# Optimization experiments

Hardware: AMD Instinct MI355X
Metric: run time of the kernel (lower is better)

## Reference

```python
import jax, jax.numpy as jnp
import numpy as np

B, N = 4, 128
INPUT_SIZE, Z_SIZE = 512, 256
D_TENSOR, N_HEADS, SEQ_LEN = 64, 8, 64
D = D_TENSOR * N_HEADS * SEQ_LEN  # 32768


def setup_inputs() -> dict:
    key = jax.random.key(0)
    ks = jax.random.split(key, 10)
    s = lambda fan_in: 1.0 / np.sqrt(fan_in)
    return {
        "x": jax.random.normal(ks[0], (B, N, INPUT_SIZE), dtype=jnp.float32),
        "z": jax.random.normal(ks[1], (B, N, Z_SIZE), dtype=jnp.float32),
        "Wq": jax.random.uniform(ks[2], (Z_SIZE, D), jnp.float32, -s(Z_SIZE), s(Z_SIZE)),
        "bq": jax.random.uniform(ks[3], (D,), jnp.float32, -s(Z_SIZE), s(Z_SIZE)),
        "Wk": jax.random.uniform(ks[4], (INPUT_SIZE, D), jnp.float32, -s(INPUT_SIZE), s(INPUT_SIZE)),
        "bk": jax.random.uniform(ks[5], (D,), jnp.float32, -s(INPUT_SIZE), s(INPUT_SIZE)),
        "Wv": jax.random.uniform(ks[6], (INPUT_SIZE, D), jnp.float32, -s(INPUT_SIZE), s(INPUT_SIZE)),
        "bv": jax.random.uniform(ks[7], (D,), jnp.float32, -s(INPUT_SIZE), s(INPUT_SIZE)),
        "Wo": jax.random.uniform(ks[8], (D, INPUT_SIZE), jnp.float32, -s(D), s(D)),
        "bo": jax.random.uniform(ks[9], (INPUT_SIZE,), jnp.float32, -s(D), s(D)),
    }


def reference(x, z, Wq, bq, Wk, bk, Wv, bv, Wo, bo):
    # Q, K, V: [B, N, heads, seq_len, d_tensor]
    Q = (z @ Wq + bq).reshape(B, N, N_HEADS, SEQ_LEN, D_TENSOR)
    K = (x @ Wk + bk).reshape(B, N, N_HEADS, SEQ_LEN, D_TENSOR)
    V = (x @ Wv + bv).reshape(B, N, N_HEADS, SEQ_LEN, D_TENSOR)
    scores = jnp.einsum("bnhqd,bnhkd->bnhqk", Q, K) / np.sqrt(D_TENSOR).astype(np.float32)
    attn = jax.nn.softmax(scores, axis=-1)
    out = jnp.einsum("bnhqk,bnhkd->bnhqd", attn, V).reshape(B, N, D)
    return out @ Wo + bo
```

## Files before the change

kernel.cpp:

```cpp
#include <hip/hip_runtime.h>
#include <stdint.h>


typedef __attribute__((ext_vector_type(8))) short short8;
typedef __attribute__((ext_vector_type(4))) float floatx4;

__device__ __forceinline__ unsigned short f2bf(float f) {
  union { float f; unsigned int u; } v; v.f = f;
  unsigned int u = v.u + 0x7FFFu + ((v.u >> 16) & 1u);
  return (unsigned short)(u >> 16);
}

__device__ __forceinline__ unsigned int cvt_pk_bf16(float lo, float hi) {
  unsigned int r;
  asm("v_cvt_pk_bf16_f32 %0, %1, %2" : "=v"(r) : "v"(lo), "v"(hi));
  return r;
}

#define MFMA16(a, b, c) __builtin_amdgcn_mfma_f32_16x16x32_bf16((a), (b), (c), 0, 0, 0)

#define STAGE_TILE(SRC, LD, LDSARR)                                            \
  do {                                                                         \
    _Pragma("unroll") for (int i_ = 0; i_ < 4; ++i_) {                         \
      int e_ = tid + (i_ << 8);                                                \
      int r_ = e_ >> 3;                                                        \
      int c_ = (e_ & 7) ^ (r_ & 7);                                            \
      __builtin_amdgcn_global_load_lds(                                        \
          (const __attribute__((address_space(1))) unsigned int*)((SRC) +      \
              (size_t)r_ * (LD) + (c_ << 3)),                                  \
          (__attribute__((address_space(3))) unsigned int*)(&(LDSARR)[e_ << 3]),\
          16, 0, 0);                                                           \
    }                                                                          \
  } while (0)

#define FRAG(LDSARR, ROW, KS)                                                  \
  (*(const short8*)(&(LDSARR)[(((ROW) << 6)) +                                 \
      ((((((KS) << 2) + quad)) ^ ((ROW) & 7)) << 3)]))

template <int LDW>
__device__ __forceinline__ void b_issue(const float* __restrict__ Wp,
                                        float* fB, int n, int octb) {
#pragma unroll
  for (int g = 0; g < 4; ++g) {
    const int oct = octb + 2 * g;
    const float* src = Wp + (size_t)(oct << 3) * LDW + n;
#pragma unroll
    for (int j = 0; j < 8; ++j) fB[g * 8 + j] = src[(size_t)j * LDW];
  }
}

__device__ __forceinline__ void b_write(unsigned short* Bs, const float* fB,
                                        int n, int octb) {
#pragma unroll
  for (int g = 0; g < 4; ++g) {
    const int oct = octb + 2 * g;
    uint4 p;
    p.x = cvt_pk_bf16(fB[g * 8 + 0], fB[g * 8 + 1]);
    p.y = cvt_pk_bf16(fB[g * 8 + 2], fB[g * 8 + 3]);
    p.z = cvt_pk_bf16(fB[g * 8 + 4], fB[g * 8 + 5]);
    p.w = cvt_pk_bf16(fB[g * 8 + 6], fB[g * 8 + 7]);
    *(uint4*)(&Bs[(n << 6) + ((oct ^ (n & 7)) << 3)]) = p;
  }
}

__global__ __launch_bounds__(256) void convert_xz(const float* __restrict__ x,
                                                  const float* __restrict__ z,
                                                  unsigned short* __restrict__ xb,
                                                  unsigned short* __restrict__ zb) {
  int idx = (blockIdx.x * 256 + threadIdx.x) * 8;
  const float* src;
  unsigned short* dst;
  if (idx < 262144) { src = x + idx; dst = xb + idx; }
  else              { src = z + (idx - 262144); dst = zb + (idx - 262144); }
  float4 f0 = *(const float4*)src;
  float4 f1 = *(const float4*)(src + 4);
  uint4 p;
  p.x = f2bf(f0.x) | ((unsigned)f2bf(f0.y) << 16);
  p.y = f2bf(f0.z) | ((unsigned)f2bf(f0.w) << 16);
  p.z = f2bf(f1.x) | ((unsigned)f2bf(f1.y) << 16);
  p.w = f2bf(f1.z) | ((unsigned)f2bf(f1.w) << 16);
  *(uint4*)dst = p;
}

__global__ __launch_bounds__(256, 2) void gemm_qkv(const unsigned short* __restrict__ xb,
                                                   const unsigned short* __restrict__ zb,
                                                   const float* __restrict__ Wq,
                                                   const float* __restrict__ Wk,
                                                   const float* __restrict__ Wv,
                                                   const float* __restrict__ bq,
                                                   const float* __restrict__ bk,
                                                   const float* __restrict__ bv,
                                                   unsigned short* __restrict__ Qb,
                                                   unsigned short* __restrict__ Kb,
                                                   unsigned short* __restrict__ Vb) {
  __shared__ __align__(16) unsigned short As[2][128 * 64];
  __shared__ __align__(16) unsigned short Bs[2][128 * 64];
  const int tid = threadIdx.x;
  const int zsel = blockIdx.z;
  const unsigned short* A;
  const float* W;
  const float* bias;
  unsigned short* C;
  int Ka;
  if (zsel == 0)      { A = zb; W = Wq; bias = bq; C = Qb; Ka = 256; }
  else if (zsel == 1) { A = xb; W = Wk; bias = bk; C = Kb; Ka = 512; }
  else                { A = xb; W = Wv; bias = bv; C = Vb; Ka = 512; }
  const int id = blockIdx.x;
  const int xcd = id & 7, bj = id >> 3;
  const int m0 = (bj & 3) << 7;
  const int n0 = ((xcd << 5) | (bj >> 2)) << 7;
  const int lane = tid & 63, wid = tid >> 6;
  const int quad = lane >> 4, l15 = lane & 15;
  const int wm = wid >> 1, wn = wid & 1;
  const int n = tid & 127;
  const int octb = __builtin_amdgcn_readfirstlane(tid >> 7);
  const int nsteps = Ka >> 6;

  float fB[32];
  floatx4 acc[4][4] = {};
  int c = 0;
  STAGE_TILE(A + (size_t)m0 * Ka, Ka, As[0]);
  b_issue<32768>(W + n0, fB, n, octb);
  for (int t = 0; t < nsteps; ++t) {
    b_write(Bs[c], fB, n, octb);
    __syncthreads();
    if (t + 1 < nsteps) {
      STAGE_TILE(A + (size_t)m0 * Ka + ((t + 1) << 6), Ka, As[c ^ 1]);
      b_issue<32768>(W + ((size_t)(t + 1) << 6) * 32768 + n0, fB, n, octb);
    }
    __builtin_amdgcn_sched_barrier(0);
#pragma unroll
    for (int ks = 0; ks < 2; ++ks) {
      short8 aF[4], bF[4];
#pragma unroll
      for (int mi = 0; mi < 4; ++mi) aF[mi] = FRAG(As[c], wm * 64 + mi * 16 + l15, ks);
#pragma unroll
      for (int ni = 0; ni < 4; ++ni) bF[ni] = FRAG(Bs[c], wn * 64 + ni * 16 + l15, ks);
#pragma unroll
      for (int mi = 0; mi < 4; ++mi)
#pragma unroll
        for (int ni = 0; ni < 4; ++ni)
          acc[mi][ni] = MFMA16(aF[mi], bF[ni], acc[mi][ni]);
    }
    c ^= 1;
  }
#pragma unroll
  for (int ni = 0; ni < 4; ++ni) {
    int col = n0 + wn * 64 + ni * 16 + l15;
    float bv2 = bias[col];
#pragma unroll
    for (int mi = 0; mi < 4; ++mi) {
      int row = m0 + wm * 64 + mi * 16 + (quad << 2);
#pragma unroll
      for (int r = 0; r < 4; ++r)
        C[(size_t)(row + r) * 32768 + col] = f2bf(acc[mi][ni][r] + bv2);
    }
  }
}

__global__ __launch_bounds__(256) void attn64(const unsigned short* __restrict__ Qb,
                                              const unsigned short* __restrict__ Kb,
                                              const unsigned short* __restrict__ Vb,
                                              unsigned short* __restrict__ Ob) {
  __shared__ __align__(16) unsigned short Qs[64 * 72];
  __shared__ __align__(16) unsigned short Ks[64 * 72];
  __shared__ __align__(16) unsigned short VT[64 * 72];
  __shared__ __align__(16) unsigned short Ps[64 * 72];
  const int tid = threadIdx.x;
  const int bn = blockIdx.x >> 3, h = blockIdx.x & 7;
  const size_t base = (size_t)bn * 32768 + (size_t)h * 4096;
  const unsigned short* q = Qb + base;
  const unsigned short* k = Kb + base;
  const unsigned short* v = Vb + base;
#pragma unroll
  for (int i = 0; i < 2; ++i) {
    int e = tid + (i << 8);
    int r = e >> 3, dblk = e & 7;
    *(uint4*)(&Qs[r * 72 + dblk * 8]) = *(const uint4*)(q + r * 64 + dblk * 8);
    *(uint4*)(&Ks[r * 72 + dblk * 8]) = *(const uint4*)(k + r * 64 + dblk * 8);
    uint4 vv = *(const uint4*)(v + r * 64 + dblk * 8);
    const unsigned short* pv = (const unsigned short*)&vv;
#pragma unroll
    for (int j = 0; j < 8; ++j)
      VT[(dblk * 8 + j) * 72 + r] = pv[j];
  }
  __syncthreads();
  const int lane = tid & 63, wid = tid >> 6;
  const int quad = lane >> 4, l15 = lane & 15;
  const int qs = wid << 4;
  short8 aq0 = *(const short8*)(&Qs[(qs + l15) * 72 + quad * 8]);
  short8 aq1 = *(const short8*)(&Qs[(qs + l15) * 72 + 32 + quad * 8]);
  floatx4 s[4] = {};
#pragma unroll
  for (int ni = 0; ni < 4; ++ni) {
    short8 b0 = *(const short8*)(&Ks[(ni * 16 + l15) * 72 + quad * 8]);
    short8 b1 = *(const short8*)(&Ks[(ni * 16 + l15) * 72 + 32 + quad * 8]);
    s[ni] = MFMA16(aq0, b0, s[ni]);
    s[ni] = MFMA16(aq1, b1, s[ni]);
  }
#pragma unroll
  for (int r = 0; r < 4; ++r) {
    float e0 = s[0][r] * 0.125f, e1 = s[1][r] * 0.125f;
    float e2 = s[2][r] * 0.125f, e3 = s[3][r] * 0.125f;
    float m = fmaxf(fmaxf(e0, e1), fmaxf(e2, e3));
    m = fmaxf(m, __shfl_xor(m, 1));
    m = fmaxf(m, __shfl_xor(m, 2));
    m = fmaxf(m, __shfl_xor(m, 4));
    m = fmaxf(m, __shfl_xor(m, 8));
    float x0 = __expf(e0 - m), x1 = __expf(e1 - m);
    float x2 = __expf(e2 - m), x3 = __expf(e3 - m);
    float t = x0 + x1 + x2 + x3;
    t += __shfl_xor(t, 1); t += __shfl_xor(t, 2);
    t += __shfl_xor(t, 4); t += __shfl_xor(t, 8);
    float inv = __builtin_amdgcn_rcpf(t);
    int row = qs + (quad << 2) + r;
    Ps[row * 72 +      l15] = f2bf(x0 * inv);
    Ps[row * 72 + 16 + l15] = f2bf(x1 * inv);
    Ps[row * 72 + 32 + l15] = f2bf(x2 * inv);
    Ps[row * 72 + 48 + l15] = f2bf(x3 * inv);
  }
  __syncthreads();
  short8 ap0 = *(const short8*)(&Ps[(qs + l15) * 72 + quad * 8]);
  short8 ap1 = *(const short8*)(&Ps[(qs + l15) * 72 + 32 + quad * 8]);
  floatx4 o[4] = {};
#pragma unroll
  for (int ni = 0; ni < 4; ++ni) {
    short8 b0 = *(const short8*)(&VT[(ni * 16 + l15) * 72 + quad * 8]);
    short8 b1 = *(const short8*)(&VT[(ni * 16 + l15) * 72 + 32 + quad * 8]);
    o[ni] = MFMA16(ap0, b0, o[ni]);
    o[ni] = MFMA16(ap1, b1, o[ni]);
  }
  unsigned short* outp = Ob + base;
#pragma unroll
  for (int ni = 0; ni < 4; ++ni)
#pragma unroll
    for (int r = 0; r < 4; ++r)
      outp[(qs + (quad << 2) + r) * 64 + ni * 16 + l15] = f2bf(o[ni][r]);
}

__global__ __launch_bounds__(256, 2) void gemm_out(const unsigned short* __restrict__ A,
                                                   const float* __restrict__ Wo,
                                                   float* __restrict__ Cp) {
  __shared__ __align__(16) unsigned short As[2][128 * 64];
  __shared__ __align__(16) unsigned short Bs[2][128 * 64];
  const int tid = threadIdx.x;
  const int id = blockIdx.x;
  const int xcd = id & 7, bj = id >> 3;
  const int m0 = (bj & 3) << 7;
  const int q = bj >> 2;
  const int n0 = (q & 3) << 7;
  const int ks = (xcd << 2) | (q >> 2);
  const int kbase = ks << 10;
  const int lane = tid & 63, wid = tid >> 6;
  const int quad = lane >> 4, l15 = lane & 15;
  const int wm = wid >> 1, wn = wid & 1;
  const int n = tid & 127;
  const int octb = __builtin_amdgcn_readfirstlane(tid >> 7);

  float fB[32];
  floatx4 acc[4][4] = {};
  int c = 0;
  STAGE_TILE(A + (size_t)m0 * 32768 + kbase, 32768, As[0]);
  b_issue<512>(Wo + (size_t)kbase * 512 + n0, fB, n, octb);
  for (int t = 0; t < 16; ++t) {
    b_write(Bs[c], fB, n, octb);
    __syncthreads();
    if (t + 1 < 16) {
      STAGE_TILE(A + (size_t)m0 * 32768 + kbase + ((t + 1) << 6), 32768, As[c ^ 1]);
      b_issue<512>(Wo + (size_t)(kbase + ((t + 1) << 6)) * 512 + n0, fB, n, octb);
    }
    __builtin_amdgcn_sched_barrier(0);
#pragma unroll
    for (int kss = 0; kss < 2; ++kss) {
      short8 aF[4], bF[4];
#pragma unroll
      for (int mi = 0; mi < 4; ++mi) aF[mi] = FRAG(As[c], wm * 64 + mi * 16 + l15, kss);
#pragma unroll
      for (int ni = 0; ni < 4; ++ni) bF[ni] = FRAG(Bs[c], wn * 64 + ni * 16 + l15, kss);
#pragma unroll
      for (int mi = 0; mi < 4; ++mi)
#pragma unroll
        for (int ni = 0; ni < 4; ++ni)
          acc[mi][ni] = MFMA16(aF[mi], bF[ni], acc[mi][ni]);
    }
    c ^= 1;
  }
  float* outp = Cp + (size_t)ks * 262144;
#pragma unroll
  for (int ni = 0; ni < 4; ++ni) {
    int col = n0 + wn * 64 + ni * 16 + l15;
#pragma unroll
    for (int mi = 0; mi < 4; ++mi) {
      int row = m0 + wm * 64 + mi * 16 + (quad << 2);
#pragma unroll
      for (int r = 0; r < 4; ++r)
        outp[(size_t)(row + r) * 512 + col] = acc[mi][ni][r];
    }
  }
}

__global__ __launch_bounds__(256) void reduce_out(const float* __restrict__ Cp,
                                                  const float* __restrict__ bias,
                                                  float* __restrict__ C) {
  int idx = blockIdx.x * 256 + threadIdx.x;
  float s = bias[idx & 511];
#pragma unroll
  for (int k = 0; k < 32; ++k) s += Cp[(size_t)k * 262144 + idx];
  C[idx] = s;
}

extern "C" void kernel_launch(void* const* d_in, const int* in_sizes, int n_in,
                              void* d_out, int out_size, void* d_ws, size_t ws_size,
                              hipStream_t stream) {
  const float* x  = (const float*)d_in[0];
  const float* z  = (const float*)d_in[1];
  const float* Wq = (const float*)d_in[2];
  const float* bq = (const float*)d_in[3];
  const float* Wk = (const float*)d_in[4];
  const float* bk = (const float*)d_in[5];
  const float* Wv = (const float*)d_in[6];
  const float* bv = (const float*)d_in[7];
  const float* Wo = (const float*)d_in[8];
  const float* bo = (const float*)d_in[9];
  float* out = (float*)d_out;
  char* ws = (char*)d_ws;

  unsigned short* Qb = (unsigned short*)(ws + 0);
  unsigned short* Kb = (unsigned short*)(ws + 33554432);
  unsigned short* Vb = (unsigned short*)(ws + 67108864);
  unsigned short* Ob = (unsigned short*)(ws + 100663296);
  unsigned short* xb = (unsigned short*)(ws + 134217728);
  unsigned short* zb = (unsigned short*)(ws + 134742016);
  float*          Cp = (float*)(ws + 135266304);

  convert_xz<<<dim3(192), 256, 0, stream>>>(x, z, xb, zb);

  gemm_qkv<<<dim3(1024, 1, 3), 256, 0, stream>>>(xb, zb, Wq, Wk, Wv,
                                                 bq, bk, bv, Qb, Kb, Vb);

  attn64<<<dim3(4096), 256, 0, stream>>>(Qb, Kb, Vb, Ob);

  gemm_out<<<dim3(512), 256, 0, stream>>>(Ob, Wo, Cp);

  reduce_out<<<dim3(1024), 256, 0, stream>>>(Cp, bo, out);
}
```

Measured before the change: 350.3 us.

## Double-buffer weight register prefetch with explicit waitcnt in both GEMMs

Both GEMM kernels now keep two register buffers of FP32 weights and prefetch the weight tile two k-steps ahead, unrolling the loop by two with static LDS buffers. Explicit s_waitcnt vmcnt/lgkmcnt plus a raw s_barrier replace __syncthreads, and sched_barriers pin the order of loads and MFMAs. The goal is to hide global weight-load latency behind MFMA work. The cost is 32 more VGPRs per thread, which could hurt occupancy under launch_bounds(256,2), and correctness now depends on the hand-written vmcnt counts matching the real number of loads.

```diff
diff --git a/kernel.cpp b/kernel.cpp
--- a/kernel.cpp
+++ b/kernel.cpp
@@ -93,8 +93,8 @@
                                                    unsigned short* __restrict__ Qb,
                                                    unsigned short* __restrict__ Kb,
                                                    unsigned short* __restrict__ Vb) {
-  __shared__ __align__(16) unsigned short As[2][128 * 64];
-  __shared__ __align__(16) unsigned short Bs[2][128 * 64];
+  __shared__ __align__(16) unsigned short As0[128 * 64], As1[128 * 64];
+  __shared__ __align__(16) unsigned short Bs0[128 * 64], Bs1[128 * 64];
   const int tid = threadIdx.x;
   const int zsel = blockIdx.z;
   const unsigned short* A;
@@ -116,33 +116,49 @@
   const int octb = __builtin_amdgcn_readfirstlane(tid >> 7);
   const int nsteps = Ka >> 6;
 
-  float fB[32];
+  float fB0[32], fB1[32];
   floatx4 acc[4][4] = {};
-  int c = 0;
-  STAGE_TILE(A + (size_t)m0 * Ka, Ka, As[0]);
-  b_issue<32768>(W + n0, fB, n, octb);
-  for (int t = 0; t < nsteps; ++t) {
-    b_write(Bs[c], fB, n, octb);
-    __syncthreads();
-    if (t + 1 < nsteps) {
-      STAGE_TILE(A + (size_t)m0 * Ka + ((t + 1) << 6), Ka, As[c ^ 1]);
-      b_issue<32768>(W + ((size_t)(t + 1) << 6) * 32768 + n0, fB, n, octb);
-    }
+
+  b_issue<32768>(W + n0, fB0, n, octb);
+  __builtin_amdgcn_sched_barrier(0);
+  STAGE_TILE(A + (size_t)m0 * Ka, Ka, As0);
+  __builtin_amdgcn_sched_barrier(0);
+  b_issue<32768>(W + (size_t)64 * 32768 + n0, fB1, n, octb);
+  __builtin_amdgcn_sched_barrier(0);
+
+  auto step = [&](int t, float (&fBc)[32], unsigned short* AsC,
+                  unsigned short* BsC, unsigned short* AsN) {
+    if (t == nsteps - 1) { asm volatile("s_waitcnt vmcnt(0)" ::: "memory"); }
+    else                 { asm volatile("s_waitcnt vmcnt(32)" ::: "memory"); }
+    __builtin_amdgcn_sched_barrier(0);
+    b_write(BsC, fBc, n, octb);
+    asm volatile("s_waitcnt lgkmcnt(0)" ::: "memory");
+    __builtin_amdgcn_s_barrier();
+    __builtin_amdgcn_sched_barrier(0);
+    if (t + 1 < nsteps)
+      STAGE_TILE(A + (size_t)m0 * Ka + ((t + 1) << 6), Ka, AsN);
     __builtin_amdgcn_sched_barrier(0);
 #pragma unroll
     for (int ks = 0; ks < 2; ++ks) {
       short8 aF[4], bF[4];
 #pragma unroll
-      for (int mi = 0; mi < 4; ++mi) aF[mi] = FRAG(As[c], wm * 64 + mi * 16 + l15, ks);
-#pragma unroll
-      for (int ni = 0; ni < 4; ++ni) bF[ni] = FRAG(Bs[c], wn * 64 + ni * 16 + l15, ks);
+      for (int mi = 0; mi < 4; ++mi) aF[mi] = FRAG(AsC, wm * 64 + mi * 16 + l15, ks);
+#pragma unroll
+      for (int ni = 0; ni < 4; ++ni) bF[ni] = FRAG(BsC, wn * 64 + ni * 16 + l15, ks);
 #pragma unroll
       for (int mi = 0; mi < 4; ++mi)
 #pragma unroll
         for (int ni = 0; ni < 4; ++ni)
           acc[mi][ni] = MFMA16(aF[mi], bF[ni], acc[mi][ni]);
     }
-    c ^= 1;
+    __builtin_amdgcn_sched_barrier(0);
+    if (t + 2 < nsteps)
+      b_issue<32768>(W + ((size_t)(t + 2) << 6) * 32768 + n0, fBc, n, octb);
+    __builtin_amdgcn_sched_barrier(0);
+  };
+  for (int t = 0; t < nsteps; t += 2) {
+    step(t,     fB0, As0, Bs0, As1);
+    step(t + 1, fB1, As1, Bs1, As0);
   }
 #pragma unroll
   for (int ni = 0; ni < 4; ++ni) {
@@ -241,8 +257,8 @@
 __global__ __launch_bounds__(256, 2) void gemm_out(const unsigned short* __restrict__ A,
                                                    const float* __restrict__ Wo,
                                                    float* __restrict__ Cp) {
-  __shared__ __align__(16) unsigned short As[2][128 * 64];
-  __shared__ __align__(16) unsigned short Bs[2][128 * 64];
+  __shared__ __align__(16) unsigned short As0[128 * 64], As1[128 * 64];
+  __shared__ __align__(16) unsigned short Bs0[128 * 64], Bs1[128 * 64];
   const int tid = threadIdx.x;
   const int id = blockIdx.x;
   const int xcd = id & 7, bj = id >> 3;
@@ -256,34 +272,51 @@
   const int wm = wid >> 1, wn = wid & 1;
   const int n = tid & 127;
   const int octb = __builtin_amdgcn_readfirstlane(tid >> 7);
-
-  float fB[32];
+  const int nsteps = 16;
+
+  float fB0[32], fB1[32];
   floatx4 acc[4][4] = {};
-  int c = 0;
-  STAGE_TILE(A + (size_t)m0 * 32768 + kbase, 32768, As[0]);
-  b_issue<512>(Wo + (size_t)kbase * 512 + n0, fB, n, octb);
-  for (int t = 0; t < 16; ++t) {
-    b_write(Bs[c], fB, n, octb);
-    __syncthreads();
-    if (t + 1 < 16) {
-      STAGE_TILE(A + (size_t)m0 * 32768 + kbase + ((t + 1) << 6), 32768, As[c ^ 1]);
-      b_issue<512>(Wo + (size_t)(kbase + ((t + 1) << 6)) * 512 + n0, fB, n, octb);
-    }
+
+  b_issue<512>(Wo + (size_t)kbase * 512 + n0, fB0, n, octb);
+  __builtin_amdgcn_sched_barrier(0);
+  STAGE_TILE(A + (size_t)m0 * 32768 + kbase, 32768, As0);
+  __builtin_amdgcn_sched_barrier(0);
+  b_issue<512>(Wo + (size_t)(kbase + 64) * 512 + n0, fB1, n, octb);
+  __builtin_amdgcn_sched_barrier(0);
+
+  auto step = [&](int t, float (&fBc)[32], unsigned short* AsC,
+                  unsigned short* BsC, unsigned short* AsN) {
+    if (t == nsteps - 1) { asm volatile("s_waitcnt vmcnt(0)" ::: "memory"); }
+    else                 { asm volatile("s_waitcnt vmcnt(32)" ::: "memory"); }
+    __builtin_amdgcn_sched_barrier(0);
+    b_write(BsC, fBc, n, octb);
+    asm volatile("s_waitcnt lgkmcnt(0)" ::: "memory");
+    __builtin_amdgcn_s_barrier();
+    __builtin_amdgcn_sched_barrier(0);
+    if (t + 1 < nsteps)
+      STAGE_TILE(A + (size_t)m0 * 32768 + kbase + ((t + 1) << 6), 32768, AsN);
     __builtin_amdgcn_sched_barrier(0);
 #pragma unroll
     for (int kss = 0; kss < 2; ++kss) {
       short8 aF[4], bF[4];
 #pragma unroll
-      for (int mi = 0; mi < 4; ++mi) aF[mi] = FRAG(As[c], wm * 64 + mi * 16 + l15, kss);
-#pragma unroll
-      for (int ni = 0; ni < 4; ++ni) bF[ni] = FRAG(Bs[c], wn * 64 + ni * 16 + l15, kss);
+      for (int mi = 0; mi < 4; ++mi) aF[mi] = FRAG(AsC, wm * 64 + mi * 16 + l15, kss);
+#pragma unroll
+      for (int ni = 0; ni < 4; ++ni) bF[ni] = FRAG(BsC, wn * 64 + ni * 16 + l15, kss);
 #pragma unroll
       for (int mi = 0; mi < 4; ++mi)
 #pragma unroll
         for (int ni = 0; ni < 4; ++ni)
           acc[mi][ni] = MFMA16(aF[mi], bF[ni], acc[mi][ni]);
     }
-    c ^= 1;
+    __builtin_amdgcn_sched_barrier(0);
+    if (t + 2 < nsteps)
+      b_issue<512>(Wo + (size_t)(kbase + ((t + 2) << 6)) * 512 + n0, fBc, n, octb);
+    __builtin_amdgcn_sched_barrier(0);
+  };
+  for (int t = 0; t < nsteps; t += 2) {
+    step(t,     fB0, As0, Bs0, As1);
+    step(t + 1, fB1, As1, Bs1, As0);
   }
   float* outp = Cp + (size_t)ks * 262144;
 #pragma unroll
```

New measurement: 346.6 us. Within noise of the previous version (-1.0%).

## Single-buffer B tile in LDS to fit three blocks per CU in GEMMs

Applied to the files above, without the earlier changes.

Both bf16 GEMM kernels drop the double-buffered B tile in LDS down to one buffer and raise launch bounds from 2 to 3 blocks per CU, so LDS use falls from 64KB to 48KB per block. A second barrier at the end of each k-step protects the single B buffer, and an explicit full vmcnt/lgkmcnt wait before the first barrier serializes outstanding loads. The aim is more resident waves to hide memory latency. The cost is an extra barrier per iteration, a global-load wait that removes some of the previous prefetch overlap, and register pressure from the tighter occupancy target (fB[32] plus 64 accumulators) that could cause spills.

```diff
diff --git a/kernel.cpp b/kernel.cpp
--- a/kernel.cpp
+++ b/kernel.cpp
@@ -82,7 +82,7 @@
   *(uint4*)dst = p;
 }
 
-__global__ __launch_bounds__(256, 2) void gemm_qkv(const unsigned short* __restrict__ xb,
+__global__ __launch_bounds__(256, 3) void gemm_qkv(const unsigned short* __restrict__ xb,
                                                    const unsigned short* __restrict__ zb,
                                                    const float* __restrict__ Wq,
                                                    const float* __restrict__ Wk,
@@ -94,7 +94,7 @@
                                                    unsigned short* __restrict__ Kb,
                                                    unsigned short* __restrict__ Vb) {
   __shared__ __align__(16) unsigned short As[2][128 * 64];
-  __shared__ __align__(16) unsigned short Bs[2][128 * 64];
+  __shared__ __align__(16) unsigned short Bs[128 * 64];
   const int tid = threadIdx.x;
   const int zsel = blockIdx.z;
   const unsigned short* A;
@@ -118,14 +118,21 @@
 
   float fB[32];
   floatx4 acc[4][4] = {};
-  int c = 0;
+
   STAGE_TILE(A + (size_t)m0 * Ka, Ka, As[0]);
+  __builtin_amdgcn_sched_barrier(0);
   b_issue<32768>(W + n0, fB, n, octb);
+  __builtin_amdgcn_sched_barrier(0);
+
   for (int t = 0; t < nsteps; ++t) {
-    b_write(Bs[c], fB, n, octb);
-    __syncthreads();
+    const int cur = t & 1;
+    b_write(Bs, fB, n, octb);
+    asm volatile("s_waitcnt vmcnt(0) lgkmcnt(0)" ::: "memory");
+    __builtin_amdgcn_s_barrier();
+    __builtin_amdgcn_sched_barrier(0);
     if (t + 1 < nsteps) {
-      STAGE_TILE(A + (size_t)m0 * Ka + ((t + 1) << 6), Ka, As[c ^ 1]);
+      STAGE_TILE(A + (size_t)m0 * Ka + ((t + 1) << 6), Ka, As[cur ^ 1]);
+      __builtin_amdgcn_sched_barrier(0);
       b_issue<32768>(W + ((size_t)(t + 1) << 6) * 32768 + n0, fB, n, octb);
     }
     __builtin_amdgcn_sched_barrier(0);
@@ -133,16 +140,16 @@
     for (int ks = 0; ks < 2; ++ks) {
       short8 aF[4], bF[4];
 #pragma unroll
-      for (int mi = 0; mi < 4; ++mi) aF[mi] = FRAG(As[c], wm * 64 + mi * 16 + l15, ks);
-#pragma unroll
-      for (int ni = 0; ni < 4; ++ni) bF[ni] = FRAG(Bs[c], wn * 64 + ni * 16 + l15, ks);
+      for (int mi = 0; mi < 4; ++mi) aF[mi] = FRAG(As[cur], wm * 64 + mi * 16 + l15, ks);
+#pragma unroll
+      for (int ni = 0; ni < 4; ++ni) bF[ni] = FRAG(Bs, wn * 64 + ni * 16 + l15, ks);
 #pragma unroll
       for (int mi = 0; mi < 4; ++mi)
 #pragma unroll
         for (int ni = 0; ni < 4; ++ni)
           acc[mi][ni] = MFMA16(aF[mi], bF[ni], acc[mi][ni]);
     }
-    c ^= 1;
+    __builtin_amdgcn_s_barrier();
   }
 #pragma unroll
   for (int ni = 0; ni < 4; ++ni) {
@@ -238,11 +245,11 @@
       outp[(qs + (quad << 2) + r) * 64 + ni * 16 + l15] = f2bf(o[ni][r]);
 }
 
-__global__ __launch_bounds__(256, 2) void gemm_out(const unsigned short* __restrict__ A,
+__global__ __launch_bounds__(256, 3) void gemm_out(const unsigned short* __restrict__ A,
                                                    const float* __restrict__ Wo,
                                                    float* __restrict__ Cp) {
   __shared__ __align__(16) unsigned short As[2][128 * 64];
-  __shared__ __align__(16) unsigned short Bs[2][128 * 64];
+  __shared__ __align__(16) unsigned short Bs[128 * 64];
   const int tid = threadIdx.x;
   const int id = blockIdx.x;
   const int xcd = id & 7, bj = id >> 3;
@@ -256,17 +263,25 @@
   const int wm = wid >> 1, wn = wid & 1;
   const int n = tid & 127;
   const int octb = __builtin_amdgcn_readfirstlane(tid >> 7);
+  const int nsteps = 16;
 
   float fB[32];
   floatx4 acc[4][4] = {};
-  int c = 0;
+
   STAGE_TILE(A + (size_t)m0 * 32768 + kbase, 32768, As[0]);
+  __builtin_amdgcn_sched_barrier(0);
   b_issue<512>(Wo + (size_t)kbase * 512 + n0, fB, n, octb);
-  for (int t = 0; t < 16; ++t) {
-    b_write(Bs[c], fB, n, octb);
-    __syncthreads();
-    if (t + 1 < 16) {
-      STAGE_TILE(A + (size_t)m0 * 32768 + kbase + ((t + 1) << 6), 32768, As[c ^ 1]);
+  __builtin_amdgcn_sched_barrier(0);
+
+  for (int t = 0; t < nsteps; ++t) {
+    const int cur = t & 1;
+    b_write(Bs, fB, n, octb);
+    asm volatile("s_waitcnt vmcnt(0) lgkmcnt(0)" ::: "memory");
+    __builtin_amdgcn_s_barrier();
+    __builtin_amdgcn_sched_barrier(0);
+    if (t + 1 < nsteps) {
+      STAGE_TILE(A + (size_t)m0 * 32768 + kbase + ((t + 1) << 6), 32768, As[cur ^ 1]);
+      __builtin_amdgcn_sched_barrier(0);
       b_issue<512>(Wo + (size_t)(kbase + ((t + 1) << 6)) * 512 + n0, fB, n, octb);
     }
     __builtin_amdgcn_sched_barrier(0);
@@ -274,16 +289,16 @@
     for (int kss = 0; kss < 2; ++kss) {
       short8 aF[4], bF[4];
 #pragma unroll
-      for (int mi = 0; mi < 4; ++mi) aF[mi] = FRAG(As[c], wm * 64 + mi * 16 + l15, kss);
-#pragma unroll
-      for (int ni = 0; ni < 4; ++ni) bF[ni] = FRAG(Bs[c], wn * 64 + ni * 16 + l15, kss);
+      for (int mi = 0; mi < 4; ++mi) aF[mi] = FRAG(As[cur], wm * 64 + mi * 16 + l15, kss);
+#pragma unroll
+      for (int ni = 0; ni < 4; ++ni) bF[ni] = FRAG(Bs, wn * 64 + ni * 16 + l15, kss);
 #pragma unroll
       for (int mi = 0; mi < 4; ++mi)
 #pragma unroll
         for (int ni = 0; ni < 4; ++ni)
           acc[mi][ni] = MFMA16(aF[mi], bF[ni], acc[mi][ni]);
     }
-    c ^= 1;
+    __builtin_amdgcn_s_barrier();
   }
   float* outp = Cp + (size_t)ks * 262144;
 #pragma unroll
```

Result: faster. 334.1 us (-4.6%).
